# Performance work log

Hardware: AMD Instinct MI355X
Metric: run time of the kernel (lower is better)

The kernel has to match this reference:

```python
import jax, jax.numpy as jnp
import numpy as np

N_NODES = 50000
IN_FEAT = 64
HIDDEN = 128
SCALAR_DIM = 64
VECTOR_DIM = 32
N_EDGES = 800000
INPUT_DIM = 3 * IN_FEAT + 1  # 193


def _mlp(x, W1, b1, W2, b2):
    # Linear -> ReLU -> Linear (make_mlp)
    h = jax.nn.relu(x @ W1 + b1)
    return h @ W2 + b2


def setup_inputs() -> dict:
    key = jax.random.key(0)
    ks = jax.random.split(key, 12)
    s = lambda fan_in: 1.0 / np.sqrt(fan_in)
    return {
        "endpoints": jax.random.randint(ks[0], (N_EDGES, 2), 0, N_NODES, dtype=jnp.int64),
        "edge_lengths": jax.random.uniform(ks[1], (N_EDGES, 1), dtype=jnp.float32),
        "midpoint_theta": jax.random.normal(ks[2], (N_EDGES,), dtype=jnp.float32),
        "endpoint_features": jax.random.normal(ks[3], (N_NODES, IN_FEAT), dtype=jnp.float32),
        "W1s": jax.random.normal(ks[4], (INPUT_DIM, HIDDEN), dtype=jnp.float32) * s(INPUT_DIM),
        "b1s": jnp.zeros((HIDDEN,), dtype=jnp.float32),
        "W2s": jax.random.normal(ks[5], (HIDDEN, SCALAR_DIM), dtype=jnp.float32) * s(HIDDEN),
        "b2s": jnp.zeros((SCALAR_DIM,), dtype=jnp.float32),
        "W1v": jax.random.normal(ks[6], (INPUT_DIM, HIDDEN), dtype=jnp.float32) * s(INPUT_DIM),
        "b1v": jnp.zeros((HIDDEN,), dtype=jnp.float32),
        "W2v": jax.random.normal(ks[7], (HIDDEN, VECTOR_DIM), dtype=jnp.float32) * s(HIDDEN),
        "b2v": jnp.zeros((VECTOR_DIM,), dtype=jnp.float32),
    }


def reference(endpoints, edge_lengths, midpoint_theta, endpoint_features,
              W1s, b1s, W2s, b2s, W1v, b1v, W2v, b2v):
    i = endpoints[:, 0]
    j = endpoints[:, 1]
    feat_i = endpoint_features[i]            # [E, F] gather
    feat_j = endpoint_features[j]            # [E, F] gather
    diff = jnp.abs(feat_i - feat_j)          # [E, F]
    inputs = jnp.concatenate([feat_i, feat_j, diff, edge_lengths], axis=-1)  # [E, 3F+1]
    h0 = _mlp(inputs, W1s, b1s, W2s, b2s)    # [E, scalar_dim]
    direction = jnp.stack([jnp.cos(midpoint_theta), jnp.sin(midpoint_theta)], axis=-1)  # [E, 2]
    amplitude = _mlp(inputs, W1v, b1v, W2v, b2v)[..., None]  # [E, vector_dim, 1]
    v0 = amplitude * direction[:, None, :]   # [E, vector_dim, 2]
    return (h0, v0)
```

## Files before the change

### kernel.cpp

```cpp
#include <hip/hip_runtime.h>
#include <hip/hip_bf16.h>

#define N_EDGES 800000
#define M_BLK   64
#define NBLK    (N_EDGES / M_BLK)
#define N_NODES 50000

typedef __attribute__((ext_vector_type(8))) _Float16 half8;
typedef __attribute__((ext_vector_type(4))) float    f32x4;

#define WS_FEAT16_OFF 131072
#define WS_NEEDED     (WS_FEAT16_OFF + (size_t)N_NODES * 64 * 2)

__global__ void prep_kernel(const float* __restrict__ W1s, const float* __restrict__ W1v,
                            const float* __restrict__ W2s, const float* __restrict__ W2v,
                            _Float16* __restrict__ wt1s, _Float16* __restrict__ wt1v,
                            _Float16* __restrict__ wt2s, _Float16* __restrict__ wt2v,
                            float* __restrict__ w1s192, float* __restrict__ w1v192)
{
    int idx = blockIdx.x * blockDim.x + threadIdx.x;
    if (idx < 128 * 192) {
        int c = idx / 192, k = idx % 192;
        wt1s[idx] = (_Float16)W1s[k * 128 + c];
        wt1v[idx] = (_Float16)W1v[k * 128 + c];
        return;
    }
    int i2 = idx - 128 * 192;
    if (i2 >= 0 && i2 < 64 * 128) {
        int c = i2 / 128, k = i2 % 128;
        wt2s[i2] = (_Float16)W2s[k * 64 + c];
        return;
    }
    int i3 = idx - (128 * 192 + 64 * 128);
    if (i3 >= 0 && i3 < 32 * 128) {
        int c = i3 / 128, k = i3 % 128;
        wt2v[i3] = (_Float16)W2v[k * 32 + c];
        return;
    }
    int i4 = idx - (128 * 192 + 64 * 128 + 32 * 128);
    if (i4 >= 0 && i4 < 128) {
        w1s192[i4] = W1s[192 * 128 + i4];
        w1v192[i4] = W1v[192 * 128 + i4];
    }
}

__global__ void prep_feat16(const float* __restrict__ feat, _Float16* __restrict__ feat16)
{
    int idx = blockIdx.x * blockDim.x + threadIdx.x;
    if (idx < N_NODES * 32) {
        float2 v = ((const float2*)feat)[idx];
        feat16[idx * 2]     = (_Float16)v.x;
        feat16[idx * 2 + 1] = (_Float16)v.y;
    }
}

__device__ __forceinline__ void* xsw(char* base, int row, int byte_in_row, int row_bytes)
{
    int chunk = byte_in_row >> 4;
    int sw    = ((chunk ^ (row & 7)) << 4) | (byte_in_row & 15);
    return (void*)(base + row * row_bytes + sw);
}

__global__ void edge_mlp_kernel(
    const int*   __restrict__ endpoints,
    const float* __restrict__ edge_len,
    const float* __restrict__ theta,
    const _Float16* __restrict__ feat16,
    const float* __restrict__ b1s, const float* __restrict__ b2s,
    const float* __restrict__ b1v, const float* __restrict__ b2v,
    const _Float16* __restrict__ wt1s, const _Float16* __restrict__ wt1v,
    const _Float16* __restrict__ wt2s, const _Float16* __restrict__ wt2v,
    const float* __restrict__ w1s192, const float* __restrict__ w1v192,
    float* __restrict__ h0, float* __restrict__ v0)
{
    __shared__ char   lds[32768];
    __shared__ float  Len[M_BLK];
    __shared__ float2 Dir[M_BLK];
    char* ldsX  = lds;
    char* ldsHs = lds;
    char* ldsHv = lds + 16384;

    const int t   = threadIdx.x;
    const int blk = blockIdx.x;
    const int w   = t >> 6;
    const int l   = t & 63;
    const int lr  = l & 15;
    const int lk  = l >> 4;
    const int e   = t >> 3;
    const int f0q = t & 7;
    const int base = blk * M_BLK;

    const int c1 = w * 16 + lr;

    {
        int2 ep0 = ((const int2*)endpoints)[base + e];
        half8 pi = *(const half8*)(feat16 + (size_t)ep0.x * 64 + f0q * 8);
        half8 pj = *(const half8*)(feat16 + (size_t)ep0.y * 64 + f0q * 8);
        half8 pd;
#pragma unroll
        for (int q = 0; q < 8; ++q) {
            _Float16 d = (_Float16)(pi[q] - pj[q]);
            pd[q] = d < (_Float16)0 ? (_Float16)(-d) : d;
        }
        *(half8*)xsw(ldsX, e, f0q * 16, 384)       = pi;
        *(half8*)xsw(ldsX, e, 128 + f0q * 16, 384) = pj;
        *(half8*)xsw(ldsX, e, 256 + f0q * 16, 384) = pd;
        if (t < M_BLK)          Len[t] = edge_len[base + t];
        else if (t < 2 * M_BLK) {
            float th = theta[base + (t - M_BLK)];
            Dir[t - M_BLK] = make_float2(cosf(th), sinf(th));
        }
    }

    const float b1s_c   = b1s[c1];
    const float b1v_c   = b1v[c1];
    const float w192s_c = w1s192[c1];
    const float w192v_c = w1v192[c1];
    const int rt2 = w >> 1;
    const int ch  = w & 1;
    const float b2s_a = b2s[ch * 32 + lr];
    const float b2s_b = b2s[ch * 32 + 16 + lr];
    const float b2v_c = b2v[ch * 16 + lr];

    __syncthreads();

    f32x4 accs[4], accv[4];
    {
        const char* pws = (const char*)wt1s + c1 * 384 + lk * 16;
        const char* pwv = (const char*)wt1v + c1 * 384 + lk * 16;
#pragma unroll
        for (int rt = 0; rt < 4; ++rt) {
            accs[rt] = (f32x4){0.f, 0.f, 0.f, 0.f};
            accv[rt] = (f32x4){0.f, 0.f, 0.f, 0.f};
        }
        half8 bs = *reinterpret_cast<const half8*>(pws);
        half8 bv = *reinterpret_cast<const half8*>(pwv);
#pragma unroll
        for (int ks = 0; ks < 6; ++ks) {
            half8 bsn = bs, bvn = bv;
            if (ks < 5) {
                bsn = *reinterpret_cast<const half8*>(pws + (ks + 1) * 64);
                bvn = *reinterpret_cast<const half8*>(pwv + (ks + 1) * 64);
            }
#pragma unroll
            for (int rt = 0; rt < 4; ++rt) {
                half8 a = *(half8*)xsw(ldsX, rt * 16 + lr, ks * 64 + lk * 16, 384);
                accs[rt] = __builtin_amdgcn_mfma_f32_16x16x32_f16(a, bs, accs[rt], 0, 0, 0);
                accv[rt] = __builtin_amdgcn_mfma_f32_16x16x32_f16(a, bv, accv[rt], 0, 0, 0);
            }
            bs = bsn; bv = bvn;
        }
    }
    __syncthreads();

#pragma unroll
    for (int rt = 0; rt < 4; ++rt) {
        float4 l4 = *reinterpret_cast<const float4*>(&Len[rt * 16 + lk * 4]);
        float lv[4] = {l4.x, l4.y, l4.z, l4.w};
#pragma unroll
        for (int r = 0; r < 4; ++r) {
            int row = rt * 16 + lk * 4 + r;
            float hs = accs[rt][r] + b1s_c + lv[r] * w192s_c;
            float hv = accv[rt][r] + b1v_c + lv[r] * w192v_c;
            *(_Float16*)xsw(ldsHs, row, c1 * 2, 256) = (_Float16)fmaxf(hs, 0.f);
            *(_Float16*)xsw(ldsHv, row, c1 * 2, 256) = (_Float16)fmaxf(hv, 0.f);
        }
    }
    __syncthreads();

    {
        f32x4 acc2[2];
        acc2[0] = (f32x4){0.f, 0.f, 0.f, 0.f};
        acc2[1] = (f32x4){0.f, 0.f, 0.f, 0.f};
        f32x4 accV = (f32x4){0.f, 0.f, 0.f, 0.f};
        const int cv = ch * 16 + lr;
#pragma unroll
        for (int ks = 0; ks < 4; ++ks) {
            half8 a2 = *(half8*)xsw(ldsHs, rt2 * 16 + lr, ks * 64 + lk * 16, 256);
#pragma unroll
            for (int ct = 0; ct < 2; ++ct) {
                int c2 = ch * 32 + ct * 16 + lr;
                half8 b = *reinterpret_cast<const half8*>(wt2s + c2 * 128 + ks * 32 + lk * 8);
                acc2[ct] = __builtin_amdgcn_mfma_f32_16x16x32_f16(a2, b, acc2[ct], 0, 0, 0);
            }
            half8 av  = *(half8*)xsw(ldsHv, rt2 * 16 + lr, ks * 64 + lk * 16, 256);
            half8 bv2 = *reinterpret_cast<const half8*>(wt2v + cv * 128 + ks * 32 + lk * 8);
            accV = __builtin_amdgcn_mfma_f32_16x16x32_f16(av, bv2, accV, 0, 0, 0);
        }
#pragma unroll
        for (int ct = 0; ct < 2; ++ct) {
            int c2 = ch * 32 + ct * 16 + lr;
            float bias = ct ? b2s_b : b2s_a;
#pragma unroll
            for (int r = 0; r < 4; ++r) {
                int row = rt2 * 16 + lk * 4 + r;
                h0[(size_t)(base + row) * 64 + c2] = acc2[ct][r] + bias;
            }
        }
#pragma unroll
        for (int r = 0; r < 4; ++r) {
            int row = rt2 * 16 + lk * 4 + r;
            float amp = accV[r] + b2v_c;
            float2 d = Dir[row];
            *reinterpret_cast<float2*>(v0 + ((size_t)(base + row) * 32 + cv) * 2) =
                make_float2(amp * d.x, amp * d.y);
        }
    }
}

__global__ void edge_mlp_kernel_f32(
    const int*   __restrict__ endpoints,
    const float* __restrict__ edge_len,
    const float* __restrict__ theta,
    const float* __restrict__ feat,
    const float* __restrict__ b1s, const float* __restrict__ b2s,
    const float* __restrict__ b1v, const float* __restrict__ b2v,
    const _Float16* __restrict__ wt1s, const _Float16* __restrict__ wt1v,
    const _Float16* __restrict__ wt2s, const _Float16* __restrict__ wt2v,
    const float* __restrict__ w1s192, const float* __restrict__ w1v192,
    float* __restrict__ h0, float* __restrict__ v0)
{
    __shared__ char   lds[32768];
    __shared__ float  Len[M_BLK];
    __shared__ float2 Dir[M_BLK];
    char* ldsX  = lds;
    char* ldsHs = lds;
    char* ldsHv = lds + 16384;

    const int t   = threadIdx.x;
    const int blk = blockIdx.x;
    const int w   = t >> 6;
    const int l   = t & 63;
    const int lr  = l & 15;
    const int lk  = l >> 4;
    const int e   = t >> 3;
    const int f0q = t & 7;
    const int base = blk * M_BLK;
    const int c1 = w * 16 + lr;

    {
        int2 ep0 = ((const int2*)endpoints)[base + e];
        const float* pfi = feat + (size_t)ep0.x * 64 + f0q * 8;
        const float* pfj = feat + (size_t)ep0.y * 64 + f0q * 8;
        float4 fi0 = ((const float4*)pfi)[0], fi1 = ((const float4*)pfi)[1];
        float4 fj0 = ((const float4*)pfj)[0], fj1 = ((const float4*)pfj)[1];
        float ai[8] = {fi0.x, fi0.y, fi0.z, fi0.w, fi1.x, fi1.y, fi1.z, fi1.w};
        float bj[8] = {fj0.x, fj0.y, fj0.z, fj0.w, fj1.x, fj1.y, fj1.z, fj1.w};
        half8 pi, pj, pd;
#pragma unroll
        for (int q = 0; q < 8; ++q) {
            pi[q] = (_Float16)ai[q];
            pj[q] = (_Float16)bj[q];
            pd[q] = (_Float16)fabsf(ai[q] - bj[q]);
        }
        *(half8*)xsw(ldsX, e, f0q * 16, 384)       = pi;
        *(half8*)xsw(ldsX, e, 128 + f0q * 16, 384) = pj;
        *(half8*)xsw(ldsX, e, 256 + f0q * 16, 384) = pd;
        if (t < M_BLK)          Len[t] = edge_len[base + t];
        else if (t < 2 * M_BLK) {
            float th = theta[base + (t - M_BLK)];
            Dir[t - M_BLK] = make_float2(cosf(th), sinf(th));
        }
    }

    const float b1s_c   = b1s[c1];
    const float b1v_c   = b1v[c1];
    const float w192s_c = w1s192[c1];
    const float w192v_c = w1v192[c1];
    const int rt2 = w >> 1;
    const int ch  = w & 1;
    const float b2s_a = b2s[ch * 32 + lr];
    const float b2s_b = b2s[ch * 32 + 16 + lr];
    const float b2v_c = b2v[ch * 16 + lr];

    __syncthreads();

    f32x4 accs[4], accv[4];
    {
        const char* pws = (const char*)wt1s + c1 * 384 + lk * 16;
        const char* pwv = (const char*)wt1v + c1 * 384 + lk * 16;
#pragma unroll
        for (int rt = 0; rt < 4; ++rt) {
            accs[rt] = (f32x4){0.f, 0.f, 0.f, 0.f};
            accv[rt] = (f32x4){0.f, 0.f, 0.f, 0.f};
        }
        half8 bs = *reinterpret_cast<const half8*>(pws);
        half8 bv = *reinterpret_cast<const half8*>(pwv);
#pragma unroll
        for (int ks = 0; ks < 6; ++ks) {
            half8 bsn = bs, bvn = bv;
            if (ks < 5) {
                bsn = *reinterpret_cast<const half8*>(pws + (ks + 1) * 64);
                bvn = *reinterpret_cast<const half8*>(pwv + (ks + 1) * 64);
            }
#pragma unroll
            for (int rt = 0; rt < 4; ++rt) {
                half8 a = *(half8*)xsw(ldsX, rt * 16 + lr, ks * 64 + lk * 16, 384);
                accs[rt] = __builtin_amdgcn_mfma_f32_16x16x32_f16(a, bs, accs[rt], 0, 0, 0);
                accv[rt] = __builtin_amdgcn_mfma_f32_16x16x32_f16(a, bv, accv[rt], 0, 0, 0);
            }
            bs = bsn; bv = bvn;
        }
    }
    __syncthreads();

#pragma unroll
    for (int rt = 0; rt < 4; ++rt) {
        float4 l4 = *reinterpret_cast<const float4*>(&Len[rt * 16 + lk * 4]);
        float lv[4] = {l4.x, l4.y, l4.z, l4.w};
#pragma unroll
        for (int r = 0; r < 4; ++r) {
            int row = rt * 16 + lk * 4 + r;
            float hs = accs[rt][r] + b1s_c + lv[r] * w192s_c;
            float hv = accv[rt][r] + b1v_c + lv[r] * w192v_c;
            *(_Float16*)xsw(ldsHs, row, c1 * 2, 256) = (_Float16)fmaxf(hs, 0.f);
            *(_Float16*)xsw(ldsHv, row, c1 * 2, 256) = (_Float16)fmaxf(hv, 0.f);
        }
    }
    __syncthreads();

    {
        f32x4 acc2[2];
        acc2[0] = (f32x4){0.f, 0.f, 0.f, 0.f};
        acc2[1] = (f32x4){0.f, 0.f, 0.f, 0.f};
        f32x4 accV = (f32x4){0.f, 0.f, 0.f, 0.f};
        const int cv = ch * 16 + lr;
#pragma unroll
        for (int ks = 0; ks < 4; ++ks) {
            half8 a2 = *(half8*)xsw(ldsHs, rt2 * 16 + lr, ks * 64 + lk * 16, 256);
#pragma unroll
            for (int ct = 0; ct < 2; ++ct) {
                int c2 = ch * 32 + ct * 16 + lr;
                half8 b = *reinterpret_cast<const half8*>(wt2s + c2 * 128 + ks * 32 + lk * 8);
                acc2[ct] = __builtin_amdgcn_mfma_f32_16x16x32_f16(a2, b, acc2[ct], 0, 0, 0);
            }
            half8 av  = *(half8*)xsw(ldsHv, rt2 * 16 + lr, ks * 64 + lk * 16, 256);
            half8 bv2 = *reinterpret_cast<const half8*>(wt2v + cv * 128 + ks * 32 + lk * 8);
            accV = __builtin_amdgcn_mfma_f32_16x16x32_f16(av, bv2, accV, 0, 0, 0);
        }
#pragma unroll
        for (int ct = 0; ct < 2; ++ct) {
            int c2 = ch * 32 + ct * 16 + lr;
            float bias = ct ? b2s_b : b2s_a;
#pragma unroll
            for (int r = 0; r < 4; ++r) {
                int row = rt2 * 16 + lk * 4 + r;
                h0[(size_t)(base + row) * 64 + c2] = acc2[ct][r] + bias;
            }
        }
#pragma unroll
        for (int r = 0; r < 4; ++r) {
            int row = rt2 * 16 + lk * 4 + r;
            float amp = accV[r] + b2v_c;
            float2 d = Dir[row];
            *reinterpret_cast<float2*>(v0 + ((size_t)(base + row) * 32 + cv) * 2) =
                make_float2(amp * d.x, amp * d.y);
        }
    }
}

extern "C" void kernel_launch(void* const* d_in, const int* in_sizes, int n_in,
                              void* d_out, int out_size, void* d_ws, size_t ws_size,
                              hipStream_t stream)
{
    const int*   endpoints = (const int*)d_in[0];
    const float* edge_len  = (const float*)d_in[1];
    const float* theta     = (const float*)d_in[2];
    const float* feat      = (const float*)d_in[3];
    const float* W1s       = (const float*)d_in[4];
    const float* b1s       = (const float*)d_in[5];
    const float* W2s       = (const float*)d_in[6];
    const float* b2s       = (const float*)d_in[7];
    const float* W1v       = (const float*)d_in[8];
    const float* b1v       = (const float*)d_in[9];
    const float* W2v       = (const float*)d_in[10];
    const float* b2v       = (const float*)d_in[11];

    char* ws = (char*)d_ws;
    _Float16* wt1s   = (_Float16*)(ws);
    _Float16* wt1v   = (_Float16*)(ws + 49152);
    _Float16* wt2s   = (_Float16*)(ws + 98304);
    _Float16* wt2v   = (_Float16*)(ws + 114688);
    float*    w1s192 = (float*)(ws + 122880);
    float*    w1v192 = (float*)(ws + 123392);
    _Float16* feat16 = (_Float16*)(ws + WS_FEAT16_OFF);

    prep_kernel<<<145, 256, 0, stream>>>(W1s, W1v, W2s, W2v,
                                         wt1s, wt1v, wt2s, wt2v, w1s192, w1v192);

    float* h0 = (float*)d_out;
    float* v0 = h0 + (size_t)N_EDGES * 64;

    if (ws_size >= WS_NEEDED) {
        prep_feat16<<<(N_NODES * 32 + 255) / 256, 256, 0, stream>>>(feat, feat16);
        edge_mlp_kernel<<<NBLK, 512, 0, stream>>>(endpoints, edge_len, theta, feat16,
                                                  b1s, b2s, b1v, b2v,
                                                  wt1s, wt1v, wt2s, wt2v,
                                                  w1s192, w1v192, h0, v0);
    } else {
        edge_mlp_kernel_f32<<<NBLK, 512, 0, stream>>>(endpoints, edge_len, theta, feat,
                                                      b1s, b2s, b1v, b2v,
                                                      wt1s, wt1v, wt2s, wt2v,
                                                      w1s192, w1v192, h0, v0);
    }
}
```

Measured before the change: 353.8 us.

## Split layer-1 GEMMs sequentially, load edge data to registers, compute direction per lane

The scalar and vector first-layer GEMMs now run one after the other instead of interleaved. The scalar hidden activations are written to a separate LDS region during the vector GEMM, which cuts live accumulator registers from 32 to 16 floats per lane. Edge lengths and theta are loaded straight into registers instead of staging through LDS, and cos/sin are computed per lane at the epilogue rather than by a subset of threads before the barrier. LDS usage rises to 40 KB per block, which may limit blocks per CU, and cos/sin are now evaluated redundantly across lanes.

```diff
diff --git a/kernel.cpp b/kernel.cpp
--- a/kernel.cpp
+++ b/kernel.cpp
@@ -73,12 +73,10 @@
     const float* __restrict__ w1s192, const float* __restrict__ w1v192,
     float* __restrict__ h0, float* __restrict__ v0)
 {
-    __shared__ char   lds[32768];
-    __shared__ float  Len[M_BLK];
-    __shared__ float2 Dir[M_BLK];
+    __shared__ char lds[40960];
     char* ldsX  = lds;
-    char* ldsHs = lds;
-    char* ldsHv = lds + 16384;
+    char* ldsHs = lds + 24576;
+    char* ldsHv = lds;
 
     const int t   = threadIdx.x;
     const int blk = blockIdx.x;
@@ -91,6 +89,14 @@
     const int base = blk * M_BLK;
 
     const int c1 = w * 16 + lr;
+    const int rt2 = w >> 1;
+    const int ch  = w & 1;
+
+    float4 len_a[4];
+#pragma unroll
+    for (int rt = 0; rt < 4; ++rt)
+        len_a[rt] = *(const float4*)(edge_len + base + rt * 16 + lk * 4);
+    float4 th4 = *(const float4*)(theta + base + rt2 * 16 + lk * 4);
 
     {
         int2 ep0 = ((const int2*)endpoints)[base + e];
@@ -99,70 +105,80 @@
         half8 pd;
 #pragma unroll
         for (int q = 0; q < 8; ++q) {
-            _Float16 d = (_Float16)(pi[q] - pj[q]);
+            _Float16 d = pi[q] - pj[q];
             pd[q] = d < (_Float16)0 ? (_Float16)(-d) : d;
         }
         *(half8*)xsw(ldsX, e, f0q * 16, 384)       = pi;
         *(half8*)xsw(ldsX, e, 128 + f0q * 16, 384) = pj;
         *(half8*)xsw(ldsX, e, 256 + f0q * 16, 384) = pd;
-        if (t < M_BLK)          Len[t] = edge_len[base + t];
-        else if (t < 2 * M_BLK) {
-            float th = theta[base + (t - M_BLK)];
-            Dir[t - M_BLK] = make_float2(cosf(th), sinf(th));
-        }
     }
 
     const float b1s_c   = b1s[c1];
     const float b1v_c   = b1v[c1];
     const float w192s_c = w1s192[c1];
     const float w192v_c = w1v192[c1];
-    const int rt2 = w >> 1;
-    const int ch  = w & 1;
     const float b2s_a = b2s[ch * 32 + lr];
     const float b2s_b = b2s[ch * 32 + 16 + lr];
     const float b2v_c = b2v[ch * 16 + lr];
 
     __syncthreads();
 
-    f32x4 accs[4], accv[4];
     {
         const char* pws = (const char*)wt1s + c1 * 384 + lk * 16;
-        const char* pwv = (const char*)wt1v + c1 * 384 + lk * 16;
-#pragma unroll
-        for (int rt = 0; rt < 4; ++rt) {
-            accs[rt] = (f32x4){0.f, 0.f, 0.f, 0.f};
-            accv[rt] = (f32x4){0.f, 0.f, 0.f, 0.f};
-        }
-        half8 bs = *reinterpret_cast<const half8*>(pws);
-        half8 bv = *reinterpret_cast<const half8*>(pwv);
+        f32x4 acc[4];
+#pragma unroll
+        for (int rt = 0; rt < 4; ++rt) acc[rt] = (f32x4){0.f, 0.f, 0.f, 0.f};
+        half8 bw = *reinterpret_cast<const half8*>(pws);
 #pragma unroll
         for (int ks = 0; ks < 6; ++ks) {
-            half8 bsn = bs, bvn = bv;
-            if (ks < 5) {
-                bsn = *reinterpret_cast<const half8*>(pws + (ks + 1) * 64);
-                bvn = *reinterpret_cast<const half8*>(pwv + (ks + 1) * 64);
-            }
+            half8 bwn = bw;
+            if (ks < 5) bwn = *reinterpret_cast<const half8*>(pws + (ks + 1) * 64);
 #pragma unroll
             for (int rt = 0; rt < 4; ++rt) {
                 half8 a = *(half8*)xsw(ldsX, rt * 16 + lr, ks * 64 + lk * 16, 384);
-                accs[rt] = __builtin_amdgcn_mfma_f32_16x16x32_f16(a, bs, accs[rt], 0, 0, 0);
-                accv[rt] = __builtin_amdgcn_mfma_f32_16x16x32_f16(a, bv, accv[rt], 0, 0, 0);
-            }
-            bs = bsn; bv = bvn;
+                acc[rt] = __builtin_amdgcn_mfma_f32_16x16x32_f16(a, bw, acc[rt], 0, 0, 0);
+            }
+            bw = bwn;
+        }
+#pragma unroll
+        for (int rt = 0; rt < 4; ++rt) {
+            float lv[4] = {len_a[rt].x, len_a[rt].y, len_a[rt].z, len_a[rt].w};
+#pragma unroll
+            for (int r = 0; r < 4; ++r) {
+                int row = rt * 16 + lk * 4 + r;
+                float hs = acc[rt][r] + b1s_c + lv[r] * w192s_c;
+                *(_Float16*)xsw(ldsHs, row, c1 * 2, 256) = (_Float16)fmaxf(hs, 0.f);
+            }
+        }
+    }
+
+    f32x4 accv[4];
+    {
+        const char* pwv = (const char*)wt1v + c1 * 384 + lk * 16;
+#pragma unroll
+        for (int rt = 0; rt < 4; ++rt) accv[rt] = (f32x4){0.f, 0.f, 0.f, 0.f};
+        half8 bw = *reinterpret_cast<const half8*>(pwv);
+#pragma unroll
+        for (int ks = 0; ks < 6; ++ks) {
+            half8 bwn = bw;
+            if (ks < 5) bwn = *reinterpret_cast<const half8*>(pwv + (ks + 1) * 64);
+#pragma unroll
+            for (int rt = 0; rt < 4; ++rt) {
+                half8 a = *(half8*)xsw(ldsX, rt * 16 + lr, ks * 64 + lk * 16, 384);
+                accv[rt] = __builtin_amdgcn_mfma_f32_16x16x32_f16(a, bw, accv[rt], 0, 0, 0);
+            }
+            bw = bwn;
         }
     }
     __syncthreads();
 
 #pragma unroll
     for (int rt = 0; rt < 4; ++rt) {
-        float4 l4 = *reinterpret_cast<const float4*>(&Len[rt * 16 + lk * 4]);
-        float lv[4] = {l4.x, l4.y, l4.z, l4.w};
+        float lv[4] = {len_a[rt].x, len_a[rt].y, len_a[rt].z, len_a[rt].w};
 #pragma unroll
         for (int r = 0; r < 4; ++r) {
             int row = rt * 16 + lk * 4 + r;
-            float hs = accs[rt][r] + b1s_c + lv[r] * w192s_c;
             float hv = accv[rt][r] + b1v_c + lv[r] * w192v_c;
-            *(_Float16*)xsw(ldsHs, row, c1 * 2, 256) = (_Float16)fmaxf(hs, 0.f);
             *(_Float16*)xsw(ldsHv, row, c1 * 2, 256) = (_Float16)fmaxf(hv, 0.f);
         }
     }
@@ -187,6 +203,12 @@
             half8 bv2 = *reinterpret_cast<const half8*>(wt2v + cv * 128 + ks * 32 + lk * 8);
             accV = __builtin_amdgcn_mfma_f32_16x16x32_f16(av, bv2, accV, 0, 0, 0);
         }
+        float dx[4], dy[4];
+        {
+            float thv[4] = {th4.x, th4.y, th4.z, th4.w};
+#pragma unroll
+            for (int r = 0; r < 4; ++r) { dx[r] = cosf(thv[r]); dy[r] = sinf(thv[r]); }
+        }
 #pragma unroll
         for (int ct = 0; ct < 2; ++ct) {
             int c2 = ch * 32 + ct * 16 + lr;
@@ -201,9 +223,8 @@
         for (int r = 0; r < 4; ++r) {
             int row = rt2 * 16 + lk * 4 + r;
             float amp = accV[r] + b2v_c;
-            float2 d = Dir[row];
             *reinterpret_cast<float2*>(v0 + ((size_t)(base + row) * 32 + cv) * 2) =
-                make_float2(amp * d.x, amp * d.y);
+                make_float2(amp * dx[r], amp * dy[r]);
         }
     }
 }
@@ -220,12 +241,10 @@
     const float* __restrict__ w1s192, const float* __restrict__ w1v192,
     float* __restrict__ h0, float* __restrict__ v0)
 {
-    __shared__ char   lds[32768];
-    __shared__ float  Len[M_BLK];
-    __shared__ float2 Dir[M_BLK];
+    __shared__ char lds[40960];
     char* ldsX  = lds;
-    char* ldsHs = lds;
-    char* ldsHv = lds + 16384;
+    char* ldsHs = lds + 24576;
+    char* ldsHv = lds;
 
     const int t   = threadIdx.x;
     const int blk = blockIdx.x;
@@ -237,6 +256,14 @@
     const int f0q = t & 7;
     const int base = blk * M_BLK;
     const int c1 = w * 16 + lr;
+    const int rt2 = w >> 1;
+    const int ch  = w & 1;
+
+    float4 len_a[4];
+#pragma unroll
+    for (int rt = 0; rt < 4; ++rt)
+        len_a[rt] = *(const float4*)(edge_len + base + rt * 16 + lk * 4);
+    float4 th4 = *(const float4*)(theta + base + rt2 * 16 + lk * 4);
 
     {
         int2 ep0 = ((const int2*)endpoints)[base + e];
@@ -256,64 +283,74 @@
         *(half8*)xsw(ldsX, e, f0q * 16, 384)       = pi;
         *(half8*)xsw(ldsX, e, 128 + f0q * 16, 384) = pj;
         *(half8*)xsw(ldsX, e, 256 + f0q * 16, 384) = pd;
-        if (t < M_BLK)          Len[t] = edge_len[base + t];
-        else if (t < 2 * M_BLK) {
-            float th = theta[base + (t - M_BLK)];
-            Dir[t - M_BLK] = make_float2(cosf(th), sinf(th));
-        }
     }
 
     const float b1s_c   = b1s[c1];
     const float b1v_c   = b1v[c1];
     const float w192s_c = w1s192[c1];
     const float w192v_c = w1v192[c1];
-    const int rt2 = w >> 1;
-    const int ch  = w & 1;
     const float b2s_a = b2s[ch * 32 + lr];
     const float b2s_b = b2s[ch * 32 + 16 + lr];
     const float b2v_c = b2v[ch * 16 + lr];
 
     __syncthreads();
 
-    f32x4 accs[4], accv[4];
     {
         const char* pws = (const char*)wt1s + c1 * 384 + lk * 16;
-        const char* pwv = (const char*)wt1v + c1 * 384 + lk * 16;
-#pragma unroll
-        for (int rt = 0; rt < 4; ++rt) {
-            accs[rt] = (f32x4){0.f, 0.f, 0.f, 0.f};
-            accv[rt] = (f32x4){0.f, 0.f, 0.f, 0.f};
-        }
-        half8 bs = *reinterpret_cast<const half8*>(pws);
-        half8 bv = *reinterpret_cast<const half8*>(pwv);
+        f32x4 acc[4];
+#pragma unroll
+        for (int rt = 0; rt < 4; ++rt) acc[rt] = (f32x4){0.f, 0.f, 0.f, 0.f};
+        half8 bw = *reinterpret_cast<const half8*>(pws);
 #pragma unroll
         for (int ks = 0; ks < 6; ++ks) {
-            half8 bsn = bs, bvn = bv;
-            if (ks < 5) {
-                bsn = *reinterpret_cast<const half8*>(pws + (ks + 1) * 64);
-                bvn = *reinterpret_cast<const half8*>(pwv + (ks + 1) * 64);
-            }
+            half8 bwn = bw;
+            if (ks < 5) bwn = *reinterpret_cast<const half8*>(pws + (ks + 1) * 64);
 #pragma unroll
             for (int rt = 0; rt < 4; ++rt) {
                 half8 a = *(half8*)xsw(ldsX, rt * 16 + lr, ks * 64 + lk * 16, 384);
-                accs[rt] = __builtin_amdgcn_mfma_f32_16x16x32_f16(a, bs, accs[rt], 0, 0, 0);
-                accv[rt] = __builtin_amdgcn_mfma_f32_16x16x32_f16(a, bv, accv[rt], 0, 0, 0);
-            }
-            bs = bsn; bv = bvn;
+                acc[rt] = __builtin_amdgcn_mfma_f32_16x16x32_f16(a, bw, acc[rt], 0, 0, 0);
+            }
+            bw = bwn;
+        }
+#pragma unroll
+        for (int rt = 0; rt < 4; ++rt) {
+            float lv[4] = {len_a[rt].x, len_a[rt].y, len_a[rt].z, len_a[rt].w};
+#pragma unroll
+            for (int r = 0; r < 4; ++r) {
+                int row = rt * 16 + lk * 4 + r;
+                float hs = acc[rt][r] + b1s_c + lv[r] * w192s_c;
+                *(_Float16*)xsw(ldsHs, row, c1 * 2, 256) = (_Float16)fmaxf(hs, 0.f);
+            }
+        }
+    }
+
+    f32x4 accv[4];
+    {
+        const char* pwv = (const char*)wt1v + c1 * 384 + lk * 16;
+#pragma unroll
+        for (int rt = 0; rt < 4; ++rt) accv[rt] = (f32x4){0.f, 0.f, 0.f, 0.f};
+        half8 bw = *reinterpret_cast<const half8*>(pwv);
+#pragma unroll
+        for (int ks = 0; ks < 6; ++ks) {
+            half8 bwn = bw;
+            if (ks < 5) bwn = *reinterpret_cast<const half8*>(pwv + (ks + 1) * 64);
+#pragma unroll
+            for (int rt = 0; rt < 4; ++rt) {
+                half8 a = *(half8*)xsw(ldsX, rt * 16 + lr, ks * 64 + lk * 16, 384);
+                accv[rt] = __builtin_amdgcn_mfma_f32_16x16x32_f16(a, bw, accv[rt], 0, 0, 0);
+            }
+            bw = bwn;
         }
     }
     __syncthreads();
 
 #pragma unroll
     for (int rt = 0; rt < 4; ++rt) {
-        float4 l4 = *reinterpret_cast<const float4*>(&Len[rt * 16 + lk * 4]);
-        float lv[4] = {l4.x, l4.y, l4.z, l4.w};
+        float lv[4] = {len_a[rt].x, len_a[rt].y, len_a[rt].z, len_a[rt].w};
 #pragma unroll
         for (int r = 0; r < 4; ++r) {
             int row = rt * 16 + lk * 4 + r;
-            float hs = accs[rt][r] + b1s_c + lv[r] * w192s_c;
             float hv = accv[rt][r] + b1v_c + lv[r] * w192v_c;
-            *(_Float16*)xsw(ldsHs, row, c1 * 2, 256) = (_Float16)fmaxf(hs, 0.f);
             *(_Float16*)xsw(ldsHv, row, c1 * 2, 256) = (_Float16)fmaxf(hv, 0.f);
         }
     }
@@ -338,6 +375,12 @@
             half8 bv2 = *reinterpret_cast<const half8*>(wt2v + cv * 128 + ks * 32 + lk * 8);
             accV = __builtin_amdgcn_mfma_f32_16x16x32_f16(av, bv2, accV, 0, 0, 0);
         }
+        float dx[4], dy[4];
+        {
+            float thv[4] = {th4.x, th4.y, th4.z, th4.w};
+#pragma unroll
+            for (int r = 0; r < 4; ++r) { dx[r] = cosf(thv[r]); dy[r] = sinf(thv[r]); }
+        }
 #pragma unroll
         for (int ct = 0; ct < 2; ++ct) {
             int c2 = ch * 32 + ct * 16 + lr;
@@ -352,9 +395,8 @@
         for (int r = 0; r < 4; ++r) {
             int row = rt2 * 16 + lk * 4 + r;
             float amp = accV[r] + b2v_c;
-            float2 d = Dir[row];
             *reinterpret_cast<float2*>(v0 + ((size_t)(base + row) * 32 + cv) * 2) =
-                make_float2(amp * d.x, amp * d.y);
+                make_float2(amp * dx[r], amp * dy[r]);
         }
     }
 }
```

Measured after the change: 343.9 us. 2.8% less time.

## Split layer-1 scalar/vector GEMMs to cut live accumulators; add separate Hs LDS buffer

Applied to the files above, without the earlier changes.

Layer 1 now computes the scalar and vector branches one after the other instead of interleaved, so only four accumulator tiles are live at a time. This lowers register pressure. The scalar hidden activations are written straight into a new dedicated LDS buffer (Hs), and the vector activations reuse the input buffer after the barrier. Weight fragments are preloaded into registers, MFMA sections are wrapped in s_setprio, and layer-2 LDS reads are hoisted ahead of the MFMAs. LDS use per block grows from 32 KB to 40 KB, which may reduce occupancy, and the input tile is now read from LDS twice.

```diff
diff --git a/kernel.cpp b/kernel.cpp
--- a/kernel.cpp
+++ b/kernel.cpp
@@ -73,12 +73,10 @@
     const float* __restrict__ w1s192, const float* __restrict__ w1v192,
     float* __restrict__ h0, float* __restrict__ v0)
 {
-    __shared__ char   lds[32768];
+    __shared__ char   ldsX [M_BLK * 384];
+    __shared__ char   ldsHs[M_BLK * 256];
     __shared__ float  Len[M_BLK];
     __shared__ float2 Dir[M_BLK];
-    char* ldsX  = lds;
-    char* ldsHs = lds;
-    char* ldsHv = lds + 16384;
 
     const int t   = threadIdx.x;
     const int blk = blockIdx.x;
@@ -99,7 +97,7 @@
         half8 pd;
 #pragma unroll
         for (int q = 0; q < 8; ++q) {
-            _Float16 d = (_Float16)(pi[q] - pj[q]);
+            _Float16 d = pi[q] - pj[q];
             pd[q] = d < (_Float16)0 ? (_Float16)(-d) : d;
         }
         *(half8*)xsw(ldsX, e, f0q * 16, 384)       = pi;
@@ -124,35 +122,59 @@
 
     __syncthreads();
 
-    f32x4 accs[4], accv[4];
     {
         const char* pws = (const char*)wt1s + c1 * 384 + lk * 16;
-        const char* pwv = (const char*)wt1v + c1 * 384 + lk * 16;
-#pragma unroll
-        for (int rt = 0; rt < 4; ++rt) {
-            accs[rt] = (f32x4){0.f, 0.f, 0.f, 0.f};
-            accv[rt] = (f32x4){0.f, 0.f, 0.f, 0.f};
-        }
-        half8 bs = *reinterpret_cast<const half8*>(pws);
-        half8 bv = *reinterpret_cast<const half8*>(pwv);
-#pragma unroll
-        for (int ks = 0; ks < 6; ++ks) {
-            half8 bsn = bs, bvn = bv;
-            if (ks < 5) {
-                bsn = *reinterpret_cast<const half8*>(pws + (ks + 1) * 64);
-                bvn = *reinterpret_cast<const half8*>(pwv + (ks + 1) * 64);
-            }
+        half8 bw[6];
+#pragma unroll
+        for (int ks = 0; ks < 6; ++ks)
+            bw[ks] = *reinterpret_cast<const half8*>(pws + ks * 64);
+        f32x4 acc[4];
+#pragma unroll
+        for (int rt = 0; rt < 4; ++rt) acc[rt] = (f32x4){0.f, 0.f, 0.f, 0.f};
+        __builtin_amdgcn_s_setprio(1);
+#pragma unroll
+        for (int ks = 0; ks < 6; ++ks)
 #pragma unroll
             for (int rt = 0; rt < 4; ++rt) {
                 half8 a = *(half8*)xsw(ldsX, rt * 16 + lr, ks * 64 + lk * 16, 384);
-                accs[rt] = __builtin_amdgcn_mfma_f32_16x16x32_f16(a, bs, accs[rt], 0, 0, 0);
-                accv[rt] = __builtin_amdgcn_mfma_f32_16x16x32_f16(a, bv, accv[rt], 0, 0, 0);
-            }
-            bs = bsn; bv = bvn;
-        }
-    }
-    __syncthreads();
-
+                acc[rt] = __builtin_amdgcn_mfma_f32_16x16x32_f16(a, bw[ks], acc[rt], 0, 0, 0);
+            }
+        __builtin_amdgcn_s_setprio(0);
+#pragma unroll
+        for (int rt = 0; rt < 4; ++rt) {
+            float4 l4 = *reinterpret_cast<const float4*>(&Len[rt * 16 + lk * 4]);
+            float lv[4] = {l4.x, l4.y, l4.z, l4.w};
+#pragma unroll
+            for (int r = 0; r < 4; ++r) {
+                int row = rt * 16 + lk * 4 + r;
+                float hs = acc[rt][r] + b1s_c + lv[r] * w192s_c;
+                *(_Float16*)xsw(ldsHs, row, c1 * 2, 256) = (_Float16)fmaxf(hs, 0.f);
+            }
+        }
+    }
+
+    f32x4 accv[4];
+    {
+        const char* pwv = (const char*)wt1v + c1 * 384 + lk * 16;
+        half8 bw[6];
+#pragma unroll
+        for (int ks = 0; ks < 6; ++ks)
+            bw[ks] = *reinterpret_cast<const half8*>(pwv + ks * 64);
+#pragma unroll
+        for (int rt = 0; rt < 4; ++rt) accv[rt] = (f32x4){0.f, 0.f, 0.f, 0.f};
+        __builtin_amdgcn_s_setprio(1);
+#pragma unroll
+        for (int ks = 0; ks < 6; ++ks)
+#pragma unroll
+            for (int rt = 0; rt < 4; ++rt) {
+                half8 a = *(half8*)xsw(ldsX, rt * 16 + lr, ks * 64 + lk * 16, 384);
+                accv[rt] = __builtin_amdgcn_mfma_f32_16x16x32_f16(a, bw[ks], accv[rt], 0, 0, 0);
+            }
+        __builtin_amdgcn_s_setprio(0);
+    }
+    __syncthreads();
+
+    char* ldsHv = ldsX;
 #pragma unroll
     for (int rt = 0; rt < 4; ++rt) {
         float4 l4 = *reinterpret_cast<const float4*>(&Len[rt * 16 + lk * 4]);
@@ -160,9 +182,7 @@
 #pragma unroll
         for (int r = 0; r < 4; ++r) {
             int row = rt * 16 + lk * 4 + r;
-            float hs = accs[rt][r] + b1s_c + lv[r] * w192s_c;
             float hv = accv[rt][r] + b1v_c + lv[r] * w192v_c;
-            *(_Float16*)xsw(ldsHs, row, c1 * 2, 256) = (_Float16)fmaxf(hs, 0.f);
             *(_Float16*)xsw(ldsHv, row, c1 * 2, 256) = (_Float16)fmaxf(hv, 0.f);
         }
     }
@@ -174,19 +194,25 @@
         acc2[1] = (f32x4){0.f, 0.f, 0.f, 0.f};
         f32x4 accV = (f32x4){0.f, 0.f, 0.f, 0.f};
         const int cv = ch * 16 + lr;
+        half8 a2[4], av[4];
 #pragma unroll
         for (int ks = 0; ks < 4; ++ks) {
-            half8 a2 = *(half8*)xsw(ldsHs, rt2 * 16 + lr, ks * 64 + lk * 16, 256);
+            a2[ks] = *(half8*)xsw(ldsHs, rt2 * 16 + lr, ks * 64 + lk * 16, 256);
+            av[ks] = *(half8*)xsw(ldsHv, rt2 * 16 + lr, ks * 64 + lk * 16, 256);
+        }
+        __builtin_amdgcn_s_setprio(1);
+#pragma unroll
+        for (int ks = 0; ks < 4; ++ks) {
 #pragma unroll
             for (int ct = 0; ct < 2; ++ct) {
                 int c2 = ch * 32 + ct * 16 + lr;
                 half8 b = *reinterpret_cast<const half8*>(wt2s + c2 * 128 + ks * 32 + lk * 8);
-                acc2[ct] = __builtin_amdgcn_mfma_f32_16x16x32_f16(a2, b, acc2[ct], 0, 0, 0);
-            }
-            half8 av  = *(half8*)xsw(ldsHv, rt2 * 16 + lr, ks * 64 + lk * 16, 256);
+                acc2[ct] = __builtin_amdgcn_mfma_f32_16x16x32_f16(a2[ks], b, acc2[ct], 0, 0, 0);
+            }
             half8 bv2 = *reinterpret_cast<const half8*>(wt2v + cv * 128 + ks * 32 + lk * 8);
-            accV = __builtin_amdgcn_mfma_f32_16x16x32_f16(av, bv2, accV, 0, 0, 0);
-        }
+            accV = __builtin_amdgcn_mfma_f32_16x16x32_f16(av[ks], bv2, accV, 0, 0, 0);
+        }
+        __builtin_amdgcn_s_setprio(0);
 #pragma unroll
         for (int ct = 0; ct < 2; ++ct) {
             int c2 = ch * 32 + ct * 16 + lr;
```

Measured after the change: 342.6 us. 1.03x faster.
